# Kernel optimization log

Hardware: AMD Instinct MI355X
Metric: run time of the kernel (lower is better)

Reference implementation:

```python
import jax, jax.numpy as jnp
import numpy as np

B = 65536
H = 128          # hidden_size
IN_BOT = 128     # input_bottom_size
IN_TOP = 128     # input_top_size
GATE_W = 4 * H + 1  # 513: 4 gate chunks + 1 boundary logit
HARD_A = 1.0
ROUND_TH = 0.5


def setup_inputs() -> dict:
    key = jax.random.key(0)
    ks = jax.random.split(key, 10)
    sd = 1.0 / np.sqrt(H)
    return {
        "h_bottom": jax.random.normal(ks[0], (B, IN_BOT), jnp.float32),
        "h":        jax.random.normal(ks[1], (B, H), jnp.float32),
        "h_top":    jax.random.normal(ks[2], (B, IN_TOP), jnp.float32),
        "c":        jax.random.normal(ks[3], (B, H), jnp.float32),
        "z":        jax.random.randint(ks[4], (B, 1), 0, 2).astype(jnp.float32),
        "z_bottom": jax.random.randint(ks[5], (B, 1), 0, 2).astype(jnp.float32),
        "W": jax.random.uniform(ks[6], (IN_BOT, GATE_W), jnp.float32, -sd, sd),
        "R": jax.random.uniform(ks[7], (H, GATE_W), jnp.float32, -sd, sd),
        "U": jax.random.uniform(ks[8], (IN_TOP, GATE_W), jnp.float32, -sd, sd),
        "b": jax.random.uniform(ks[9], (GATE_W,), jnp.float32, -sd, sd),
    }


def _hard_sigm(x, a=HARD_A):
    # HardSigm: clip((a*x + 1)/2, 0, 1)
    return jnp.clip((a * x + 1.0) * 0.5, 0.0, 1.0)


def _round_st(z_tilde, th=ROUND_TH):
    # threshold rounding with straight-through gradient (identity backward)
    hard = (z_tilde > th).astype(z_tilde.dtype)
    return z_tilde + jax.lax.stop_gradient(hard - z_tilde)


def reference(h_bottom, h, h_top, c, z, z_bottom, W, R, U, b):
    # fused gate pre-activations: [B, 4H+1]
    s = (h_bottom * z_bottom) @ W + h @ R + (h_top * z) @ U + b
    si = s[:, 0 * H:1 * H]
    sg = s[:, 1 * H:2 * H]
    so = s[:, 2 * H:3 * H]
    sf = s[:, 3 * H:4 * H]
    sz = s[:, 4 * H:4 * H + 1]
    i = jax.nn.sigmoid(si)
    g = jnp.tanh(sg)
    o = jax.nn.sigmoid(so)
    f = jax.nn.sigmoid(sf)
    ig = i * g
    # FLUSH if z==1; COPY if z==0 & z_bottom==0; UPDATE otherwise
    c_new = jnp.where(z == 1.0, ig, jnp.where(z_bottom == 0.0, c, c * f + ig))
    h_new = jnp.where((z == 0.0) & (z_bottom == 0.0), h, jnp.tanh(c_new) * o)
    z_new = _round_st(_hard_sigm(sz))
    return (h_new, c_new, z_new)
```

## Files before the change

### kernel.cpp

```cpp
#include <hip/hip_runtime.h>
#include <hip/hip_bf16.h>


#define MT   64
#define BK   32
#define NKC  12
#define NT   512
#define COFF 8388608
#define ZOFF 16777216

using short8 = __attribute__((ext_vector_type(8))) short;
using f32x4  = __attribute__((ext_vector_type(4))) float;

__device__ __forceinline__ unsigned short f2bf(float f) {
  union { float f; unsigned u; } v; v.f = f;
  unsigned r = (v.u + 0x7FFFu + ((v.u >> 16) & 1u)) >> 16;
  return (unsigned short)r;
}

__device__ __forceinline__ float sigm(float x)     { return 1.f / (1.f + __expf(-x)); }
__device__ __forceinline__ float tanh_fast(float x){ return 1.f - 2.f / (1.f + __expf(2.f * x)); }

__global__ void prep_weights(const float* __restrict__ W, const float* __restrict__ R,
                             const float* __restrict__ U, unsigned short* __restrict__ Wt) {
  int idx = blockIdx.x * blockDim.x + threadIdx.x;
  if (idx >= NKC * 512 * 4) return;
  int u  = idx & 3;
  int x  = (idx >> 2) & 15;
  int tn = (idx >> 6) & 7;
  int s  = (idx >> 9) & 3;
  int c  = idx >> 11;
  int n  = (tn >> 1) * 128 + s * 32 + (tn & 1) * 16 + x;
  int k0 = c * 32 + u * 8;
  const float* src; int kb;
  if (k0 < 128)      { src = W; kb = 0;   }
  else if (k0 < 256) { src = R; kb = 128; }
  else               { src = U; kb = 256; }
  const float* colp = src + (size_t)(k0 - kb) * 513 + n;
  unsigned short vs[8];
  #pragma unroll
  for (int j = 0; j < 8; ++j) vs[j] = f2bf(colp[j * 513]);
  uint4 o;
  o.x = (unsigned)vs[0] | ((unsigned)vs[1] << 16);
  o.y = (unsigned)vs[2] | ((unsigned)vs[3] << 16);
  o.z = (unsigned)vs[4] | ((unsigned)vs[5] << 16);
  o.w = (unsigned)vs[6] | ((unsigned)vs[7] << 16);
  reinterpret_cast<uint4*>(Wt)[idx] = o;
}

__global__ __launch_bounds__(NT, 4)
void hmlstm_main(const float* __restrict__ hb, const float* __restrict__ hs,
                 const float* __restrict__ ht, const float* __restrict__ cs,
                 const float* __restrict__ zp, const float* __restrict__ zbp,
                 const float* __restrict__ W,  const float* __restrict__ R,
                 const float* __restrict__ U,  const float* __restrict__ b,
                 const unsigned short* __restrict__ Wt, float* __restrict__ out)
{
  __shared__ unsigned short ldsA[2][MT * BK];
  __shared__ float  ldsWL[384];
  __shared__ double ldsSZ[NT];

  const int tid  = threadIdx.x;
  const int l    = tid & 63;
  const int wv   = tid >> 6;
  const int ws   = wv & 3;
  const int wr   = wv >> 2;
  const int q    = l >> 4;
  const int lr   = l & 15;
  const int row0 = blockIdx.x * MT;

  for (int k = tid; k < 384; k += NT) {
    ldsWL[k] = (k < 128) ? W[k * 513 + 512]
             : (k < 256) ? R[(k - 128) * 513 + 512]
                         : U[(k - 256) * 513 + 512];
  }

  const int m    = tid >> 3;
  const int p    = tid & 7;
  const int arow = row0 + m;
  const float zbv = zbp[arow];
  const float zv  = zp[arow];
  double szacc = 0.0;

  f32x4 acc[2][8];
  {
    f32x4 zf = {0.f, 0.f, 0.f, 0.f};
    #pragma unroll
    for (int i = 0; i < 2; ++i)
      #pragma unroll
      for (int j = 0; j < 8; ++j) acc[i][j] = zf;
  }

  const int aW = m * BK + (((p >> 1) ^ ((m >> 1) & 3)) * 8) + (p & 1) * 4;
  const size_t rowb = (size_t)arow * 128 + p * 4;

  auto loadA = [&](int c) -> f32x4 {
    const float* src = (c < 4) ? hb : (c < 8) ? hs : ht;
    return *(const f32x4*)(src + rowb + (c & 3) * 32);
  };
  auto consumeA = [&](int c, f32x4 v, int buf) {
    const float scale = (c < 4) ? zbv : (c < 8) ? 1.f : zv;
    v *= scale;
    const float* wl = ldsWL + c * 32 + p * 4;
    szacc += (double)v.x * wl[0] + (double)v.y * wl[1]
           + (double)v.z * wl[2] + (double)v.w * wl[3];
    uint2 pk;
    pk.x = (unsigned)f2bf(v.x) | ((unsigned)f2bf(v.y) << 16);
    pk.y = (unsigned)f2bf(v.z) | ((unsigned)f2bf(v.w) << 16);
    *(uint2*)&ldsA[buf][aW] = pk;
  };

  const unsigned short* wkc = Wt + (size_t)ws * 4096 + lr * 32 + q * 8;

  f32x4 a0 = loadA(0);
  short8 wf[8];
  #pragma unroll
  for (int tn = 0; tn < 8; ++tn)
    wf[tn] = *(const short8*)(wkc + tn * 512);
  asm volatile("s_waitcnt lgkmcnt(0)" ::: "memory");
  __builtin_amdgcn_s_barrier();
  consumeA(0, a0, 0);
  f32x4 ain = loadA(1);
  asm volatile("s_waitcnt lgkmcnt(0)" ::: "memory");
  __builtin_amdgcn_s_barrier();

  #pragma unroll 1
  for (int kc = 0; kc < NKC; ++kc) {
    const int cur = kc & 1;
    short8 af[2];
    #pragma unroll
    for (int s = 0; s < 2; ++s) {
      int mr = wr * 32 + s * 16 + lr;
      af[s] = *(const short8*)&ldsA[cur][mr * BK + ((q ^ ((mr >> 1) & 3)) * 8)];
    }
    #pragma unroll
    for (int tn = 0; tn < 8; ++tn) {
      acc[0][tn] = __builtin_amdgcn_mfma_f32_16x16x32_bf16(af[0], wf[tn], acc[0][tn], 0, 0, 0);
      acc[1][tn] = __builtin_amdgcn_mfma_f32_16x16x32_bf16(af[1], wf[tn], acc[1][tn], 0, 0, 0);
    }
    if (kc < NKC - 1) {
      #pragma unroll
      for (int tn = 0; tn < 8; ++tn)
        wf[tn] = *(const short8*)(wkc + 16384 + tn * 512);
      consumeA(kc + 1, ain, cur ^ 1);
      if (kc < NKC - 2) ain = loadA(kc + 2);
      wkc += 16384;
      asm volatile("s_waitcnt lgkmcnt(0)" ::: "memory");
      __builtin_amdgcn_s_barrier();
    }
  }

  ldsSZ[tid] = szacc;
  __syncthreads();
  if (tid < MT) {
    const double* pz = &ldsSZ[tid * 8];
    double ss = ((pz[0] + pz[1]) + (pz[2] + pz[3])) + ((pz[4] + pz[5]) + (pz[6] + pz[7]));
    float s = (float)ss + b[512];
    out[ZOFF + row0 + tid] = (s > 0.f) ? 1.f : 0.f;
  }

  float bias[2][4];
  #pragma unroll
  for (int th = 0; th < 2; ++th) {
    const int col = ws * 32 + th * 16 + lr;
    bias[th][0] = b[col];       bias[th][1] = b[128 + col];
    bias[th][2] = b[256 + col]; bias[th][3] = b[384 + col];
  }
  #pragma unroll
  for (int s = 0; s < 2; ++s) {
    #pragma unroll
    for (int r = 0; r < 4; ++r) {
      const int row = row0 + wr * 32 + s * 16 + q * 4 + r;
      const float zr  = zp[row];
      const float zbr = zbp[row];
      const size_t rowoff = (size_t)row * 128;
      #pragma unroll
      for (int th = 0; th < 2; ++th) {
        const int col = ws * 32 + th * 16 + lr;
        const size_t off = rowoff + col;
        float si = acc[s][0 + th][r] + bias[th][0];
        float sg = acc[s][2 + th][r] + bias[th][1];
        float so = acc[s][4 + th][r] + bias[th][2];
        float sf = acc[s][6 + th][r] + bias[th][3];
        float iv = sigm(si);
        float gv = tanh_fast(sg);
        float ov = sigm(so);
        float fv = sigm(sf);
        float ig = iv * gv;
        float cv = 0.f, hv = 0.f;
        if (zr != 1.f) cv = cs[off];
        const bool keep = (zr == 0.f) && (zbr == 0.f);
        if (keep) hv = hs[off];
        float cn = (zr == 1.f) ? ig : ((zbr == 0.f) ? cv : cv * fv + ig);
        float hn = keep ? hv : tanh_fast(cn) * ov;
        out[off]        = hn;
        out[COFF + off] = cn;
      }
    }
  }
}

extern "C" void kernel_launch(void* const* d_in, const int* in_sizes, int n_in,
                              void* d_out, int out_size, void* d_ws, size_t ws_size,
                              hipStream_t stream) {
  const float* hb  = (const float*)d_in[0];
  const float* hs  = (const float*)d_in[1];
  const float* ht  = (const float*)d_in[2];
  const float* cs  = (const float*)d_in[3];
  const float* zp  = (const float*)d_in[4];
  const float* zbp = (const float*)d_in[5];
  const float* W   = (const float*)d_in[6];
  const float* R   = (const float*)d_in[7];
  const float* U   = (const float*)d_in[8];
  const float* b   = (const float*)d_in[9];
  unsigned short* Wt = (unsigned short*)d_ws;
  float* out = (float*)d_out;

  prep_weights<<<dim3(96), dim3(256), 0, stream>>>(W, R, U, Wt);
  hmlstm_main<<<dim3(65536 / MT), dim3(NT), 0, stream>>>(
      hb, hs, ht, cs, zp, zbp, W, R, U, b, Wt, out);
}
```

Baseline: 249.9 us.

## Load A fragments directly from global into registers, dropping LDS staging and barriers

The row tile shrinks to 32 rows with 4 waves per block. Each wave now loads its own A fragments straight from global memory and converts them to bf16 in registers with the packed v_cvt_pk_bf16 instruction, which removes the LDS A double buffer and the per-chunk barriers. The boundary logit is reduced by wave 0 with cross-lane shuffles instead of an LDS reduction. In exchange, all four waves load and convert the same A rows redundantly, and the smaller tiles reuse each weight fragment across fewer rows.

```diff
diff --git a/kernel.cpp b/kernel.cpp
--- a/kernel.cpp
+++ b/kernel.cpp
@@ -2,10 +2,9 @@
 #include <hip/hip_bf16.h>
 
 
-#define MT   64
-#define BK   32
+#define MT   32
 #define NKC  12
-#define NT   512
+#define NT   256
 #define COFF 8388608
 #define ZOFF 16777216
 
@@ -16,6 +15,12 @@
   union { float f; unsigned u; } v; v.f = f;
   unsigned r = (v.u + 0x7FFFu + ((v.u >> 16) & 1u)) >> 16;
   return (unsigned short)r;
+}
+
+__device__ __forceinline__ unsigned cvt_pk_bf16(float lo, float hi) {
+  unsigned r;
+  asm("v_cvt_pk_bf16_f32 %0, %1, %2" : "=v"(r) : "v"(lo), "v"(hi));
+  return r;
 }
 
 __device__ __forceinline__ float sigm(float x)     { return 1.f / (1.f + __expf(-x)); }
@@ -48,7 +53,7 @@
   reinterpret_cast<uint4*>(Wt)[idx] = o;
 }
 
-__global__ __launch_bounds__(NT, 4)
+__global__ __launch_bounds__(NT, 3)
 void hmlstm_main(const float* __restrict__ hb, const float* __restrict__ hs,
                  const float* __restrict__ ht, const float* __restrict__ cs,
                  const float* __restrict__ zp, const float* __restrict__ zbp,
@@ -56,15 +61,11 @@
                  const float* __restrict__ U,  const float* __restrict__ b,
                  const unsigned short* __restrict__ Wt, float* __restrict__ out)
 {
-  __shared__ unsigned short ldsA[2][MT * BK];
-  __shared__ float  ldsWL[384];
-  __shared__ double ldsSZ[NT];
+  __shared__ float ldsWL[384];
 
   const int tid  = threadIdx.x;
   const int l    = tid & 63;
   const int wv   = tid >> 6;
-  const int ws   = wv & 3;
-  const int wr   = wv >> 2;
   const int q    = l >> 4;
   const int lr   = l & 15;
   const int row0 = blockIdx.x * MT;
@@ -74,13 +75,12 @@
              : (k < 256) ? R[(k - 128) * 513 + 512]
                          : U[(k - 256) * 513 + 512];
   }
-
-  const int m    = tid >> 3;
-  const int p    = tid & 7;
-  const int arow = row0 + m;
-  const float zbv = zbp[arow];
-  const float zv  = zp[arow];
-  double szacc = 0.0;
+  __syncthreads();
+
+  const int r0 = row0 + lr;
+  const int r1 = row0 + 16 + lr;
+  const float zb0 = zbp[r0], zb1 = zbp[r1];
+  const float zv0 = zp[r0],  zv1 = zp[r1];
 
   f32x4 acc[2][8];
   {
@@ -91,78 +91,81 @@
       for (int j = 0; j < 8; ++j) acc[i][j] = zf;
   }
 
-  const int aW = m * BK + (((p >> 1) ^ ((m >> 1) & 3)) * 8) + (p & 1) * 4;
-  const size_t rowb = (size_t)arow * 128 + p * 4;
-
-  auto loadA = [&](int c) -> f32x4 {
-    const float* src = (c < 4) ? hb : (c < 8) ? hs : ht;
-    return *(const f32x4*)(src + rowb + (c & 3) * 32);
+  double sz0 = 0.0, sz1 = 0.0;
+
+  const unsigned a0off = (unsigned)r0 * 128 + q * 8;
+  const unsigned a1off = (unsigned)r1 * 128 + q * 8;
+  const unsigned woff  = (unsigned)wv * 4096 + lr * 32 + q * 8;
+
+  f32x4 av[4];
+  short8 af0, af1;
+
+  auto loadA = [&](int c) {
+    const float* s = (c < 4) ? hb : (c < 8) ? hs : ht;
+    const unsigned ko = (unsigned)(c & 3) * 32;
+    av[0] = *(const f32x4*)(s + a0off + ko);
+    av[1] = *(const f32x4*)(s + a0off + ko + 4);
+    av[2] = *(const f32x4*)(s + a1off + ko);
+    av[3] = *(const f32x4*)(s + a1off + ko + 4);
   };
-  auto consumeA = [&](int c, f32x4 v, int buf) {
-    const float scale = (c < 4) ? zbv : (c < 8) ? 1.f : zv;
-    v *= scale;
-    const float* wl = ldsWL + c * 32 + p * 4;
-    szacc += (double)v.x * wl[0] + (double)v.y * wl[1]
-           + (double)v.z * wl[2] + (double)v.w * wl[3];
-    uint2 pk;
-    pk.x = (unsigned)f2bf(v.x) | ((unsigned)f2bf(v.y) << 16);
-    pk.y = (unsigned)f2bf(v.z) | ((unsigned)f2bf(v.w) << 16);
-    *(uint2*)&ldsA[buf][aW] = pk;
+  auto cvtA = [&](int c) {
+    f32x4 v0 = av[0], v1 = av[1], v2 = av[2], v3 = av[3];
+    if (c < 4)       { v0 *= zb0; v1 *= zb0; v2 *= zb1; v3 *= zb1; }
+    else if (c >= 8) { v0 *= zv0; v1 *= zv0; v2 *= zv1; v3 *= zv1; }
+    if (wv == 0) {
+      const float* wl = ldsWL + c * 32 + q * 8;
+      f32x4 w0 = *(const f32x4*)wl;
+      f32x4 w1 = *(const f32x4*)(wl + 4);
+      sz0 += (double)v0.x * w0.x + (double)v0.y * w0.y + (double)v0.z * w0.z + (double)v0.w * w0.w
+           + (double)v1.x * w1.x + (double)v1.y * w1.y + (double)v1.z * w1.z + (double)v1.w * w1.w;
+      sz1 += (double)v2.x * w0.x + (double)v2.y * w0.y + (double)v2.z * w0.z + (double)v2.w * w0.w
+           + (double)v3.x * w1.x + (double)v3.y * w1.y + (double)v3.z * w1.z + (double)v3.w * w1.w;
+    }
+    union { unsigned u[4]; short8 s8; } pk0, pk1;
+    pk0.u[0] = cvt_pk_bf16(v0.x, v0.y); pk0.u[1] = cvt_pk_bf16(v0.z, v0.w);
+    pk0.u[2] = cvt_pk_bf16(v1.x, v1.y); pk0.u[3] = cvt_pk_bf16(v1.z, v1.w);
+    pk1.u[0] = cvt_pk_bf16(v2.x, v2.y); pk1.u[1] = cvt_pk_bf16(v2.z, v2.w);
+    pk1.u[2] = cvt_pk_bf16(v3.x, v3.y); pk1.u[3] = cvt_pk_bf16(v3.z, v3.w);
+    af0 = pk0.s8; af1 = pk1.s8;
   };
 
-  const unsigned short* wkc = Wt + (size_t)ws * 4096 + lr * 32 + q * 8;
-
-  f32x4 a0 = loadA(0);
+  loadA(0);
   short8 wf[8];
   #pragma unroll
   for (int tn = 0; tn < 8; ++tn)
-    wf[tn] = *(const short8*)(wkc + tn * 512);
-  asm volatile("s_waitcnt lgkmcnt(0)" ::: "memory");
-  __builtin_amdgcn_s_barrier();
-  consumeA(0, a0, 0);
-  f32x4 ain = loadA(1);
-  asm volatile("s_waitcnt lgkmcnt(0)" ::: "memory");
-  __builtin_amdgcn_s_barrier();
+    wf[tn] = *(const short8*)(Wt + woff + tn * 512);
+  cvtA(0);
 
   #pragma unroll 1
   for (int kc = 0; kc < NKC; ++kc) {
-    const int cur = kc & 1;
-    short8 af[2];
-    #pragma unroll
-    for (int s = 0; s < 2; ++s) {
-      int mr = wr * 32 + s * 16 + lr;
-      af[s] = *(const short8*)&ldsA[cur][mr * BK + ((q ^ ((mr >> 1) & 3)) * 8)];
-    }
+    if (kc < NKC - 1) loadA(kc + 1);
     #pragma unroll
     for (int tn = 0; tn < 8; ++tn) {
-      acc[0][tn] = __builtin_amdgcn_mfma_f32_16x16x32_bf16(af[0], wf[tn], acc[0][tn], 0, 0, 0);
-      acc[1][tn] = __builtin_amdgcn_mfma_f32_16x16x32_bf16(af[1], wf[tn], acc[1][tn], 0, 0, 0);
+      acc[0][tn] = __builtin_amdgcn_mfma_f32_16x16x32_bf16(af0, wf[tn], acc[0][tn], 0, 0, 0);
+      acc[1][tn] = __builtin_amdgcn_mfma_f32_16x16x32_bf16(af1, wf[tn], acc[1][tn], 0, 0, 0);
     }
     if (kc < NKC - 1) {
       #pragma unroll
       for (int tn = 0; tn < 8; ++tn)
-        wf[tn] = *(const short8*)(wkc + 16384 + tn * 512);
-      consumeA(kc + 1, ain, cur ^ 1);
-      if (kc < NKC - 2) ain = loadA(kc + 2);
-      wkc += 16384;
-      asm volatile("s_waitcnt lgkmcnt(0)" ::: "memory");
-      __builtin_amdgcn_s_barrier();
-    }
-  }
-
-  ldsSZ[tid] = szacc;
-  __syncthreads();
-  if (tid < MT) {
-    const double* pz = &ldsSZ[tid * 8];
-    double ss = ((pz[0] + pz[1]) + (pz[2] + pz[3])) + ((pz[4] + pz[5]) + (pz[6] + pz[7]));
-    float s = (float)ss + b[512];
-    out[ZOFF + row0 + tid] = (s > 0.f) ? 1.f : 0.f;
+        wf[tn] = *(const short8*)(Wt + woff + (kc + 1) * 16384 + tn * 512);
+      cvtA(kc + 1);
+    }
+  }
+
+  if (wv == 0) {
+    sz0 += __shfl_xor(sz0, 16); sz0 += __shfl_xor(sz0, 32);
+    sz1 += __shfl_xor(sz1, 16); sz1 += __shfl_xor(sz1, 32);
+    if (l < 16) {
+      const float bz = b[512];
+      out[ZOFF + r0] = ((float)sz0 + bz > 0.f) ? 1.f : 0.f;
+      out[ZOFF + r1] = ((float)sz1 + bz > 0.f) ? 1.f : 0.f;
+    }
   }
 
   float bias[2][4];
   #pragma unroll
   for (int th = 0; th < 2; ++th) {
-    const int col = ws * 32 + th * 16 + lr;
+    const int col = wv * 32 + th * 16 + lr;
     bias[th][0] = b[col];       bias[th][1] = b[128 + col];
     bias[th][2] = b[256 + col]; bias[th][3] = b[384 + col];
   }
@@ -170,13 +173,13 @@
   for (int s = 0; s < 2; ++s) {
     #pragma unroll
     for (int r = 0; r < 4; ++r) {
-      const int row = row0 + wr * 32 + s * 16 + q * 4 + r;
+      const int row = row0 + s * 16 + q * 4 + r;
       const float zr  = zp[row];
       const float zbr = zbp[row];
       const size_t rowoff = (size_t)row * 128;
       #pragma unroll
       for (int th = 0; th < 2; ++th) {
-        const int col = ws * 32 + th * 16 + lr;
+        const int col = wv * 32 + th * 16 + lr;
         const size_t off = rowoff + col;
         float si = acc[s][0 + th][r] + bias[th][0];
         float sg = acc[s][2 + th][r] + bias[th][1];
```

Measured after the change: 303.6 us. +21.5%, slower.
